# Performance work log

Hardware: AMD Instinct MI355X
Metric: run time of the kernel (lower is better)

## Reference

```python
import jax, jax.numpy as jnp
import numpy as np

NU, NI, E, DIN, D, NB, NC = 100000, 50000, 2000000, 64, 64, 2, 5


def setup_inputs() -> dict:
    key = jax.random.key(0)
    ks = jax.random.split(key, 10)
    return {
        "ufeat": jax.random.normal(ks[0], (NU, DIN), dtype=jnp.float32),
        "ifeat": jax.random.normal(ks[1], (NI, DIN), dtype=jnp.float32),
        "c_u": jax.random.uniform(ks[2], (NU, 1), dtype=jnp.float32),
        "c_i": jax.random.uniform(ks[3], (NI, 1), dtype=jnp.float32),
        "W_user": jax.random.normal(ks[4], (DIN, D), dtype=jnp.float32) * (1.0 / np.sqrt(DIN)),
        "W_item": jax.random.normal(ks[5], (DIN, D), dtype=jnp.float32) * (1.0 / np.sqrt(DIN)),
        "P": jax.random.normal(ks[6], (NB, D, D), dtype=jnp.float32) * (1.0 / np.sqrt(D)),
        "Wc": jax.random.normal(ks[7], (NC, NB), dtype=jnp.float32),
        "src": jax.random.randint(ks[8], (E,), 0, NU, dtype=jnp.int32),
        "dst": jax.random.randint(ks[9], (E,), 0, NI, dtype=jnp.int32),
    }


def reference(ufeat, ifeat, c_u, c_i, W_user, W_item, P, Wc, src, dst):
    # --- GCMCGraphConv user->item: feat @ W, scale by c_j, copy_u + sum scatter, scale by c_i ---
    msg_u = (ufeat @ W_user) * c_u                                   # [NU, D]
    h_item = jax.ops.segment_sum(msg_u[src], dst, num_segments=ifeat.shape[0]) * c_i  # [NI, D]
    # --- GCMCGraphConv item->user (reverse edges) ---
    msg_i = (ifeat @ W_item) * c_i                                   # [NI, D]
    h_user = jax.ops.segment_sum(msg_i[dst], src, num_segments=ufeat.shape[0]) * c_u  # [NU, D]
    # --- BiDecoder: per-edge bilinear dot for each basis, then basis combine ---
    hu_b = jnp.einsum('nd,sde->nse', h_user, P)                      # [NU, NB, D]
    sr = jnp.einsum('esd,ed->es', hu_b[src], h_item[dst])            # [E, NB]
    out = sr @ Wc.T                                                  # [E, NC]
    return out
```

## Files before the change

kernel.cpp:

```cpp
#include <hip/hip_runtime.h>
#include <hip/hip_fp16.h>

#define NUu 100000
#define NIi 50000
#define NEe 2000000

#define NCBI   25
#define NCBU   49
#define NCB    74
#define NBLK1  500
#define CHUNK1 4000

#define BR    16
#define NBKI  3125
#define NBKU  6250
#define CAPI  896
#define CAPU  512
#define FSUB2 8
#define FOWN2 16
#define FPC   128

__global__ __launch_bounds__(256) void gemm64_both(
    const float* __restrict__ ufeat, const float* __restrict__ ifeat,
    const float* __restrict__ W_user, const float* __restrict__ W_item,
    const float* __restrict__ c_u, const float* __restrict__ c_i,
    __half* __restrict__ msg_u, __half* __restrict__ msg_i)
{
    __shared__ float Wl[64 * 64];
    __shared__ float rows[16][64];
    const int tid  = threadIdx.x;
    const int user = (blockIdx.x < (NUu + 15) / 16) ? 1 : 0;
    const int bid  = user ? blockIdx.x : blockIdx.x - (NUu + 15) / 16;
    const float* feat = user ? ufeat : ifeat;
    const float* W    = user ? W_user : W_item;
    const float* cvec = user ? c_u : c_i;
    __half* out       = user ? msg_u : msg_i;
    const int N       = user ? NUu : NIi;

    for (int i = tid; i < 4096; i += 256) Wl[i] = W[i];
    const int r0 = bid * 16;
    for (int i = tid; i < 16 * 64; i += 256) {
        int r = r0 + (i >> 6);
        rows[i >> 6][i & 63] = (r < N) ? feat[(size_t)r * 64 + (i & 63)] : 0.f;
    }
    __syncthreads();
    const int col = tid & 63;
    const int rq  = tid >> 6;
    for (int rr = rq; rr < 16; rr += 4) {
        int r = r0 + rr;
        if (r >= N) continue;
        float s = 0.f;
        #pragma unroll
        for (int k = 0; k < 64; ++k)
            s = fmaf(rows[rr][k], Wl[k * 64 + col], s);
        out[(size_t)r * 64 + col] = __float2half(s * cvec[r]);
    }
}

__global__ __launch_bounds__(256) void hist1(
    const int* __restrict__ src, const int* __restrict__ dst, int* __restrict__ counts)
{
    __shared__ int cnt[NCB];
    const int tid = threadIdx.x;
    if (tid < NCB) cnt[tid] = 0;
    __syncthreads();
    const int beg = blockIdx.x * CHUNK1;
    for (int i = beg + tid * 4; i < beg + CHUNK1; i += 1024) {
        uint4 s4 = *(const uint4*)(src + i);
        uint4 d4 = *(const uint4*)(dst + i);
        atomicAdd(&cnt[d4.x >> 11], 1);
        atomicAdd(&cnt[d4.y >> 11], 1);
        atomicAdd(&cnt[d4.z >> 11], 1);
        atomicAdd(&cnt[d4.w >> 11], 1);
        atomicAdd(&cnt[NCBI + (s4.x >> 11)], 1);
        atomicAdd(&cnt[NCBI + (s4.y >> 11)], 1);
        atomicAdd(&cnt[NCBI + (s4.z >> 11)], 1);
        atomicAdd(&cnt[NCBI + (s4.w >> 11)], 1);
    }
    __syncthreads();
    if (tid < NCB) counts[tid * NBLK1 + blockIdx.x] = cnt[tid];
}

__global__ __launch_bounds__(256) void scan1(
    const int* __restrict__ counts, int* __restrict__ slotbase, int* __restrict__ rowptrC)
{
    __shared__ int tot[NCB], base[NCB];
    const int tid = threadIdx.x;
    if (tid < NCB) {
        int s = 0;
        for (int b = 0; b < NBLK1; ++b) s += counts[tid * NBLK1 + b];
        tot[tid] = s;
    }
    __syncthreads();
    if (tid == 0) {
        int run = 0;
        for (int c = 0; c < NCB; ++c) { base[c] = run; rowptrC[c] = run; run += tot[c]; }
        rowptrC[NCB] = run;
    }
    __syncthreads();
    if (tid < NCB) {
        int run = base[tid];
        for (int b = 0; b < NBLK1; ++b) {
            slotbase[tid * NBLK1 + b] = run;
            run += counts[tid * NBLK1 + b];
        }
    }
}

__global__ __launch_bounds__(256) void fill1(
    const int* __restrict__ src, const int* __restrict__ dst,
    const int* __restrict__ slotbase, unsigned int* __restrict__ payC)
{
    __shared__ int cur[NCB];
    const int tid = threadIdx.x;
    if (tid < NCB) cur[tid] = slotbase[tid * NBLK1 + blockIdx.x];
    __syncthreads();
    const int beg = blockIdx.x * CHUNK1;
#define F1_PROC(ss, dd)                                                     \
    {                                                                       \
        int _s = (int)(ss), _d = (int)(dd);                                 \
        int p1 = atomicAdd(&cur[_d >> 11], 1);                              \
        payC[p1] = ((unsigned)(_d & 2047) << 17) | (unsigned)_s;            \
        int p2 = atomicAdd(&cur[NCBI + (_s >> 11)], 1);                     \
        payC[p2] = ((unsigned)(_s & 2047) << 16) | (unsigned)_d;            \
    }
    for (int i = beg + tid * 4; i < beg + CHUNK1; i += 1024) {
        uint4 s4 = *(const uint4*)(src + i);
        uint4 d4 = *(const uint4*)(dst + i);
        F1_PROC(s4.x, d4.x);
        F1_PROC(s4.y, d4.y);
        F1_PROC(s4.z, d4.z);
        F1_PROC(s4.w, d4.w);
    }
#undef F1_PROC
}

__global__ __launch_bounds__(256) void fine_split2(
    const unsigned int* __restrict__ payC, const int* __restrict__ rowptrC,
    unsigned int* __restrict__ payI, int* __restrict__ cntFI,
    unsigned int* __restrict__ payU, int* __restrict__ cntFU)
{
    __shared__ int cur[FOWN2];
    const int tid = threadIdx.x;
    int bid = blockIdx.x;
    const int user = (bid >= NCBI * FSUB2) ? 1 : 0;
    if (user) bid -= NCBI * FSUB2;
    const int cbl = bid / FSUB2;
    const int sub = bid % FSUB2;
    const int c   = user ? (NCBI + cbl) : cbl;
    const int CAP = user ? CAPU : CAPI;
    unsigned int* __restrict__ payF = user ? payU : payI;
    int*          __restrict__ cntF = user ? cntFU : cntFI;

    if (tid < FOWN2) cur[tid] = 0;
    __syncthreads();

    const int beg = rowptrC[c], end = rowptrC[c + 1];
    const int a    = min(end, beg + ((4 - (beg & 3)) & 3));
    const int vend = a + ((end - a) & ~3);

#define FS_PROC(u)                                                          \
    {                                                                       \
        unsigned int _u = (u);                                              \
        int lr  = user ? (int)(_u >> 16) : (int)(_u >> 17);                 \
        int fbl = lr >> 4;                                                  \
        if ((fbl >> 4) == sub) {                                            \
            int pos = atomicAdd(&cur[fbl & 15], 1);                         \
            if (pos < CAP) {                                                \
                unsigned int g = user ? (_u & 0xffffu) : (_u & 0x1ffffu);   \
                payF[(size_t)(cbl * FPC + fbl) * CAP + pos] =               \
                    ((unsigned)(lr & 15) << 17) | g;                        \
            }                                                               \
        }                                                                   \
    }

    if (tid < a - beg) FS_PROC(payC[beg + tid]);
    for (int i = a + tid * 4; i < vend; i += 1024) {
        uint4 v = *(const uint4*)(payC + i);
        FS_PROC(v.x); FS_PROC(v.y); FS_PROC(v.z); FS_PROC(v.w);
    }
    {
        int i = vend + tid;
        if (i < end) FS_PROC(payC[i]);
    }
#undef FS_PROC

    __syncthreads();
    if (tid < FOWN2)
        cntF[cbl * FPC + sub * FOWN2 + tid] = min(cur[tid], CAP);
}

__global__ __launch_bounds__(256) void seg_both(
    const unsigned int* __restrict__ payI, const int* __restrict__ cntFI,
    const __half* __restrict__ msg_u, const float* __restrict__ c_i,
    __half2* __restrict__ h_item,
    const unsigned int* __restrict__ payU, const int* __restrict__ cntFU,
    const __half* __restrict__ msg_i, const float* __restrict__ c_u,
    __half2* __restrict__ h_user)
{
    __shared__ unsigned int sorted[CAPI];
    __shared__ float acc[BR * 64];
    __shared__ int cnt16w[4][BR];
    const int tid  = threadIdx.x;
    const int wv   = tid >> 6;
    const int user = (blockIdx.x >= NBKI) ? 1 : 0;
    const int buk  = user ? (blockIdx.x - NBKI) : blockIdx.x;
    const int CAP  = user ? CAPU : CAPI;
    const int len  = min((user ? cntFU : cntFI)[buk], CAP);
    const unsigned int* bp = (user ? payU : payI) + (size_t)buk * CAP;
    const __half2* msg2    = (const __half2*)(user ? msg_i : msg_u);
    const float* cvec      = user ? c_u : c_i;
    __half2* hout          = user ? h_user : h_item;
    const int N            = user ? NUu : NIi;

    for (int i = tid; i < BR * 64; i += 256) acc[i] = 0.f;
    if (tid < 64) ((int*)cnt16w)[tid] = 0;
    __syncthreads();
    for (int i = tid; i < len; i += 256)
        atomicAdd(&cnt16w[wv][bp[i] >> 17], 1);
    __syncthreads();
    if (tid == 0) {
        int run = 0;
        #pragma unroll
        for (int r = 0; r < BR; ++r)
            for (int w = 0; w < 4; ++w) {
                int cw = cnt16w[w][r];
                cnt16w[w][r] = run;
                run += cw;
            }
    }
    __syncthreads();
    for (int i = tid; i < len; i += 256) {
        unsigned int p = bp[i];
        int pos = atomicAdd(&cnt16w[wv][p >> 17], 1);
        sorted[pos] = p;
    }
    __syncthreads();

    const int col2  = tid & 31;
    const int half  = (tid >> 5) & 1;
    const int sid   = wv * 2 + half;
    const int chunk = (len + 7) >> 3;
    const int lo = sid * chunk;
    const int hi = min(lo + chunk, len);
    float2 facc = make_float2(0.f, 0.f);
    int crow = -1;
    for (int i = lo; i < hi; i += 8) {
        unsigned int pk[8];
        float2 vk[8];
        #pragma unroll
        for (int k = 0; k < 8; ++k)
            pk[k] = sorted[min(i + k, hi - 1)];
        #pragma unroll
        for (int k = 0; k < 8; ++k)
            vk[k] = __half22float2(msg2[(size_t)(pk[k] & 0x1ffffu) * 32 + col2]);
        #pragma unroll
        for (int k = 0; k < 8; ++k) {
            if (i + k < hi) {
                int r = (int)(pk[k] >> 17);
                if (r != crow) {
                    if (crow >= 0) {
                        atomicAdd(&acc[crow * 64 + 2 * col2],     facc.x);
                        atomicAdd(&acc[crow * 64 + 2 * col2 + 1], facc.y);
                    }
                    crow = r;
                    facc = make_float2(0.f, 0.f);
                }
                facc.x += vk[k].x;
                facc.y += vk[k].y;
            }
        }
    }
    if (crow >= 0) {
        atomicAdd(&acc[crow * 64 + 2 * col2],     facc.x);
        atomicAdd(&acc[crow * 64 + 2 * col2 + 1], facc.y);
    }
    __syncthreads();

    const int r0 = buk * BR;
    for (int idx = tid; idx < BR * 32; idx += 256) {
        int r = idx >> 5, j2 = idx & 31;
        int R = r0 + r;
        if (R < N) {
            float c = cvec[R];
            hout[(size_t)R * 32 + j2] =
                __floats2half2_rn(acc[r * 64 + 2 * j2] * c, acc[r * 64 + 2 * j2 + 1] * c);
        }
    }
}

__global__ __launch_bounds__(256) void basis_projT_h(
    const __half* __restrict__ h, const float* __restrict__ P,
    __half* __restrict__ hb, int N)
{
    __shared__ float Pl[2 * 64 * 65];
    __shared__ float rows[8][64];
    const int tid = threadIdx.x;
    for (int i = tid; i < 8192; i += 256) {
        int b = i >> 12, rem = i & 4095, dg = rem >> 6, kg = rem & 63;
        Pl[b * 4160 + kg * 65 + dg] = P[i];
    }
    const int r0 = blockIdx.x * 8;
    for (int i = tid; i < 512; i += 256) {
        int r = r0 + (i >> 6);
        rows[i >> 6][i & 63] = (r < N) ? __half2float(h[(size_t)r * 64 + (i & 63)]) : 0.f;
    }
    __syncthreads();
    const int col = tid & 63;
    const int b   = (tid >> 6) & 1;
    const int rh  = tid >> 7;
    for (int rr = rh; rr < 8; rr += 2) {
        int r = r0 + rr;
        if (r >= N) continue;
        float s = 0.f;
        #pragma unroll
        for (int k = 0; k < 64; ++k)
            s = fmaf(rows[rr][k], Pl[b * 4160 + k * 65 + col], s);
        hb[((size_t)r * 2 + b) * 64 + col] = __float2half(s);
    }
}

__global__ __launch_bounds__(256) void edge_out_h(
    const uint4* __restrict__ hu,
    const uint4* __restrict__ hib,
    const int* __restrict__ src, const int* __restrict__ dst,
    const float* __restrict__ Wc, float* __restrict__ out, int nocts)
{
    const int l   = threadIdx.x & 63;
    const int q   = l >> 3;
    const int j   = l & 7;
    const int wid = blockIdx.x * 4 + (threadIdx.x >> 6);
    const int nw  = gridDim.x * 4;
    const float wcA = (j < 5) ? Wc[2 * j]     : 0.f;
    const float wcB = (j < 5) ? Wc[2 * j + 1] : 0.f;
    for (int t = wid; t < nocts; t += nw) {
        int e = t * 8 + q;
        int s = src[e], d = dst[e];
        uint4 ua = hu[(size_t)s * 8 + j];
        uint4 b0 = hib[(size_t)d * 16 + j];
        uint4 b1 = hib[(size_t)d * 16 + 8 + j];
        float2 u0 = __half22float2(*(const __half2*)&ua.x);
        float2 u1 = __half22float2(*(const __half2*)&ua.y);
        float2 u2 = __half22float2(*(const __half2*)&ua.z);
        float2 u3 = __half22float2(*(const __half2*)&ua.w);
        float2 v0 = __half22float2(*(const __half2*)&b0.x);
        float2 v1 = __half22float2(*(const __half2*)&b0.y);
        float2 v2 = __half22float2(*(const __half2*)&b0.z);
        float2 v3 = __half22float2(*(const __half2*)&b0.w);
        float2 w0 = __half22float2(*(const __half2*)&b1.x);
        float2 w1 = __half22float2(*(const __half2*)&b1.y);
        float2 w2 = __half22float2(*(const __half2*)&b1.z);
        float2 w3 = __half22float2(*(const __half2*)&b1.w);
        float p0 = u0.x * v0.x + u0.y * v0.y + u1.x * v1.x + u1.y * v1.y
                 + u2.x * v2.x + u2.y * v2.y + u3.x * v3.x + u3.y * v3.y;
        float p1 = u0.x * w0.x + u0.y * w0.y + u1.x * w1.x + u1.y * w1.y
                 + u2.x * w2.x + u2.y * w2.y + u3.x * w3.x + u3.y * w3.y;
        #pragma unroll
        for (int m = 1; m < 8; m <<= 1) {
            p0 += __shfl_xor(p0, m, 64);
            p1 += __shfl_xor(p1, m, 64);
        }
        if (j < 5) out[(size_t)e * 5 + j] = p0 * wcA + p1 * wcB;
    }
}

extern "C" void kernel_launch(void* const* d_in, const int* in_sizes, int n_in,
                              void* d_out, int out_size, void* d_ws, size_t ws_size,
                              hipStream_t stream) {
    const float* ufeat  = (const float*)d_in[0];
    const float* ifeat  = (const float*)d_in[1];
    const float* c_u    = (const float*)d_in[2];
    const float* c_i    = (const float*)d_in[3];
    const float* W_user = (const float*)d_in[4];
    const float* W_item = (const float*)d_in[5];
    const float* P      = (const float*)d_in[6];
    const float* Wc     = (const float*)d_in[7];
    const int*   src    = (const int*)d_in[8];
    const int*   dst    = (const int*)d_in[9];
    float* out = (float*)d_out;
    char*  ws  = (char*)d_ws;

    __half*       msg_u    = (__half*)(ws);
    __half*       msg_i    = (__half*)(ws + 12800000);
    __half*       h_item   = (__half*)(ws + 19200000);
    __half*       h_user   = (__half*)(ws + 25600000);
    unsigned int* payC     = (unsigned int*)(ws + 38400000);
    __half*       hi_b     = (__half*)(ws + 38400000);
    unsigned int* payI     = (unsigned int*)(ws + 54400000);
    unsigned int* payU     = (unsigned int*)(ws + 65600000);
    int*          counts   = (int*)(ws + 78400000);
    int*          slotbase = (int*)(ws + 78551552);
    int*          rowptrC  = (int*)(ws + 78703104);
    int*          cntFI    = (int*)(ws + 78703404);
    int*          cntFU    = (int*)(ws + 78716204);

    gemm64_both<<<(NUu + 15) / 16 + (NIi + 15) / 16, 256, 0, stream>>>(
        ufeat, ifeat, W_user, W_item, c_u, c_i, msg_u, msg_i);

    hist1<<<NBLK1, 256, 0, stream>>>(src, dst, counts);
    scan1<<<1, 256, 0, stream>>>(counts, slotbase, rowptrC);
    fill1<<<NBLK1, 256, 0, stream>>>(src, dst, slotbase, payC);
    fine_split2<<<(NCBI + NCBU) * FSUB2, 256, 0, stream>>>(
        payC, rowptrC, payI, cntFI, payU, cntFU);

    seg_both<<<NBKI + NBKU, 256, 0, stream>>>(
        payI, cntFI, msg_u, c_i, (__half2*)h_item,
        payU, cntFU, msg_i, c_u, (__half2*)h_user);

    basis_projT_h<<<(NIi + 7) / 8, 256, 0, stream>>>(h_item, P, hi_b, NIi);
    edge_out_h<<<2048, 256, 0, stream>>>(
        (const uint4*)h_user, (const uint4*)hi_b, src, dst, Wc, out, NEe / 8);
}
```

Baseline: 404.6 us.

## Fuse histogram into GEMM launch, use finer coarse buckets, widen seg gathers

The edge histogram now runs in extra blocks appended to the feature GEMM launch, which removes one kernel launch and lets the two run side by side. The coarse bucket width drops from 2048 to 512 rows, so the fine split needs no sub-block filtering and each block handles a whole coarse bucket in a single pass with 32 counters. The segment-sum gather loads 4 halves (uint2) per thread across 16 streams instead of 2 halves across 8, making each load wider. The trade-offs are a larger scan (294 buckets, run serially by one block), more shared-memory atomics per row flush, and fine-split blocks that each process more edges.

Result: slower. 424.7 us (+5.0%).

```diff
diff --git a/kernel.cpp b/kernel.cpp
--- a/kernel.cpp
+++ b/kernel.cpp
@@ -5,30 +5,55 @@
 #define NIi 50000
 #define NEe 2000000
 
-#define NCBI   25
-#define NCBU   49
-#define NCB    74
+#define NCBI3  98
+#define NCBU3  196
+#define NCB3   294
 #define NBLK1  500
 #define CHUNK1 4000
+#define NGB    9375
 
 #define BR    16
 #define NBKI  3125
 #define NBKU  6250
 #define CAPI  896
 #define CAPU  512
-#define FSUB2 8
-#define FOWN2 16
-#define FPC   128
-
-__global__ __launch_bounds__(256) void gemm64_both(
+#define FPC3  32
+
+__global__ __launch_bounds__(256) void gemm_hist(
     const float* __restrict__ ufeat, const float* __restrict__ ifeat,
     const float* __restrict__ W_user, const float* __restrict__ W_item,
     const float* __restrict__ c_u, const float* __restrict__ c_i,
-    __half* __restrict__ msg_u, __half* __restrict__ msg_i)
+    __half* __restrict__ msg_u, __half* __restrict__ msg_i,
+    const int* __restrict__ src, const int* __restrict__ dst,
+    int* __restrict__ counts)
 {
     __shared__ float Wl[64 * 64];
     __shared__ float rows[16][64];
-    const int tid  = threadIdx.x;
+    __shared__ int cnt[NCB3];
+    const int tid = threadIdx.x;
+
+    if (blockIdx.x >= NGB) {
+        const int hb = blockIdx.x - NGB;
+        for (int i = tid; i < NCB3; i += 256) cnt[i] = 0;
+        __syncthreads();
+        const int beg = hb * CHUNK1;
+        for (int i = beg + tid * 4; i < beg + CHUNK1; i += 1024) {
+            uint4 s4 = *(const uint4*)(src + i);
+            uint4 d4 = *(const uint4*)(dst + i);
+            atomicAdd(&cnt[d4.x >> 9], 1);
+            atomicAdd(&cnt[d4.y >> 9], 1);
+            atomicAdd(&cnt[d4.z >> 9], 1);
+            atomicAdd(&cnt[d4.w >> 9], 1);
+            atomicAdd(&cnt[NCBI3 + (s4.x >> 9)], 1);
+            atomicAdd(&cnt[NCBI3 + (s4.y >> 9)], 1);
+            atomicAdd(&cnt[NCBI3 + (s4.z >> 9)], 1);
+            atomicAdd(&cnt[NCBI3 + (s4.w >> 9)], 1);
+        }
+        __syncthreads();
+        for (int i = tid; i < NCB3; i += 256) counts[i * NBLK1 + hb] = cnt[i];
+        return;
+    }
+
     const int user = (blockIdx.x < (NUu + 15) / 16) ? 1 : 0;
     const int bid  = user ? blockIdx.x : blockIdx.x - (NUu + 15) / 16;
     const float* feat = user ? ufeat : ifeat;
@@ -57,36 +82,12 @@
     }
 }
 
-__global__ __launch_bounds__(256) void hist1(
-    const int* __restrict__ src, const int* __restrict__ dst, int* __restrict__ counts)
-{
-    __shared__ int cnt[NCB];
+__global__ __launch_bounds__(512) void scan1(
+    const int* __restrict__ counts, int* __restrict__ slotbase, int* __restrict__ rowptrC)
+{
+    __shared__ int tot[NCB3], base[NCB3];
     const int tid = threadIdx.x;
-    if (tid < NCB) cnt[tid] = 0;
-    __syncthreads();
-    const int beg = blockIdx.x * CHUNK1;
-    for (int i = beg + tid * 4; i < beg + CHUNK1; i += 1024) {
-        uint4 s4 = *(const uint4*)(src + i);
-        uint4 d4 = *(const uint4*)(dst + i);
-        atomicAdd(&cnt[d4.x >> 11], 1);
-        atomicAdd(&cnt[d4.y >> 11], 1);
-        atomicAdd(&cnt[d4.z >> 11], 1);
-        atomicAdd(&cnt[d4.w >> 11], 1);
-        atomicAdd(&cnt[NCBI + (s4.x >> 11)], 1);
-        atomicAdd(&cnt[NCBI + (s4.y >> 11)], 1);
-        atomicAdd(&cnt[NCBI + (s4.z >> 11)], 1);
-        atomicAdd(&cnt[NCBI + (s4.w >> 11)], 1);
-    }
-    __syncthreads();
-    if (tid < NCB) counts[tid * NBLK1 + blockIdx.x] = cnt[tid];
-}
-
-__global__ __launch_bounds__(256) void scan1(
-    const int* __restrict__ counts, int* __restrict__ slotbase, int* __restrict__ rowptrC)
-{
-    __shared__ int tot[NCB], base[NCB];
-    const int tid = threadIdx.x;
-    if (tid < NCB) {
+    if (tid < NCB3) {
         int s = 0;
         for (int b = 0; b < NBLK1; ++b) s += counts[tid * NBLK1 + b];
         tot[tid] = s;
@@ -94,11 +95,11 @@
     __syncthreads();
     if (tid == 0) {
         int run = 0;
-        for (int c = 0; c < NCB; ++c) { base[c] = run; rowptrC[c] = run; run += tot[c]; }
-        rowptrC[NCB] = run;
-    }
-    __syncthreads();
-    if (tid < NCB) {
+        for (int c = 0; c < NCB3; ++c) { base[c] = run; rowptrC[c] = run; run += tot[c]; }
+        rowptrC[NCB3] = run;
+    }
+    __syncthreads();
+    if (tid < NCB3) {
         int run = base[tid];
         for (int b = 0; b < NBLK1; ++b) {
             slotbase[tid * NBLK1 + b] = run;
@@ -111,18 +112,18 @@
     const int* __restrict__ src, const int* __restrict__ dst,
     const int* __restrict__ slotbase, unsigned int* __restrict__ payC)
 {
-    __shared__ int cur[NCB];
+    __shared__ int cur[NCB3];
     const int tid = threadIdx.x;
-    if (tid < NCB) cur[tid] = slotbase[tid * NBLK1 + blockIdx.x];
+    for (int i = tid; i < NCB3; i += 256) cur[i] = slotbase[i * NBLK1 + blockIdx.x];
     __syncthreads();
     const int beg = blockIdx.x * CHUNK1;
 #define F1_PROC(ss, dd)                                                     \
     {                                                                       \
         int _s = (int)(ss), _d = (int)(dd);                                 \
-        int p1 = atomicAdd(&cur[_d >> 11], 1);                              \
-        payC[p1] = ((unsigned)(_d & 2047) << 17) | (unsigned)_s;            \
-        int p2 = atomicAdd(&cur[NCBI + (_s >> 11)], 1);                     \
-        payC[p2] = ((unsigned)(_s & 2047) << 16) | (unsigned)_d;            \
+        int p1 = atomicAdd(&cur[_d >> 9], 1);                               \
+        payC[p1] = ((unsigned)(_d & 511) << 17) | (unsigned)_s;             \
+        int p2 = atomicAdd(&cur[NCBI3 + (_s >> 9)], 1);                     \
+        payC[p2] = ((unsigned)(_s & 511) << 17) | (unsigned)_d;             \
     }
     for (int i = beg + tid * 4; i < beg + CHUNK1; i += 1024) {
         uint4 s4 = *(const uint4*)(src + i);
@@ -135,43 +136,35 @@
 #undef F1_PROC
 }
 
-__global__ __launch_bounds__(256) void fine_split2(
+__global__ __launch_bounds__(256) void fine_split3(
     const unsigned int* __restrict__ payC, const int* __restrict__ rowptrC,
     unsigned int* __restrict__ payI, int* __restrict__ cntFI,
     unsigned int* __restrict__ payU, int* __restrict__ cntFU)
 {
-    __shared__ int cur[FOWN2];
+    __shared__ int cur[FPC3];
     const int tid = threadIdx.x;
-    int bid = blockIdx.x;
-    const int user = (bid >= NCBI * FSUB2) ? 1 : 0;
-    if (user) bid -= NCBI * FSUB2;
-    const int cbl = bid / FSUB2;
-    const int sub = bid % FSUB2;
-    const int c   = user ? (NCBI + cbl) : cbl;
-    const int CAP = user ? CAPU : CAPI;
+    const int user = (blockIdx.x >= NCBI3) ? 1 : 0;
+    const int cbl  = user ? blockIdx.x - NCBI3 : blockIdx.x;
+    const int CAP  = user ? CAPU : CAPI;
     unsigned int* __restrict__ payF = user ? payU : payI;
     int*          __restrict__ cntF = user ? cntFU : cntFI;
 
-    if (tid < FOWN2) cur[tid] = 0;
-    __syncthreads();
-
-    const int beg = rowptrC[c], end = rowptrC[c + 1];
+    if (tid < FPC3) cur[tid] = 0;
+    __syncthreads();
+
+    const int beg = rowptrC[blockIdx.x], end = rowptrC[blockIdx.x + 1];
     const int a    = min(end, beg + ((4 - (beg & 3)) & 3));
     const int vend = a + ((end - a) & ~3);
 
 #define FS_PROC(u)                                                          \
     {                                                                       \
         unsigned int _u = (u);                                              \
-        int lr  = user ? (int)(_u >> 16) : (int)(_u >> 17);                 \
+        int lr  = (int)(_u >> 17);                                          \
         int fbl = lr >> 4;                                                  \
-        if ((fbl >> 4) == sub) {                                            \
-            int pos = atomicAdd(&cur[fbl & 15], 1);                         \
-            if (pos < CAP) {                                                \
-                unsigned int g = user ? (_u & 0xffffu) : (_u & 0x1ffffu);   \
-                payF[(size_t)(cbl * FPC + fbl) * CAP + pos] =               \
-                    ((unsigned)(lr & 15) << 17) | g;                        \
-            }                                                               \
-        }                                                                   \
+        int pos = atomicAdd(&cur[fbl], 1);                                  \
+        if (pos < CAP)                                                      \
+            payF[(size_t)(cbl * FPC3 + fbl) * CAP + pos] =                  \
+                ((unsigned)(lr & 15) << 17) | (_u & 0x1ffffu);              \
     }
 
     if (tid < a - beg) FS_PROC(payC[beg + tid]);
@@ -186,8 +179,8 @@
 #undef FS_PROC
 
     __syncthreads();
-    if (tid < FOWN2)
-        cntF[cbl * FPC + sub * FOWN2 + tid] = min(cur[tid], CAP);
+    if (tid < FPC3)
+        cntF[cbl * FPC3 + tid] = min(cur[tid], CAP);
 }
 
 __global__ __launch_bounds__(256) void seg_both(
@@ -208,7 +201,7 @@
     const int CAP  = user ? CAPU : CAPI;
     const int len  = min((user ? cntFU : cntFI)[buk], CAP);
     const unsigned int* bp = (user ? payU : payI) + (size_t)buk * CAP;
-    const __half2* msg2    = (const __half2*)(user ? msg_i : msg_u);
+    const uint2* msg4      = (const uint2*)(user ? msg_i : msg_u);
     const float* cvec      = user ? c_u : c_i;
     __half2* hout          = user ? h_user : h_item;
     const int N            = user ? NUu : NIi;
@@ -237,43 +230,47 @@
     }
     __syncthreads();
 
-    const int col2  = tid & 31;
-    const int half  = (tid >> 5) & 1;
-    const int sid   = wv * 2 + half;
-    const int chunk = (len + 7) >> 3;
+    const int colq  = tid & 15;
+    const int sid   = tid >> 4;
+    const int chunk = (len + 15) >> 4;
     const int lo = sid * chunk;
     const int hi = min(lo + chunk, len);
-    float2 facc = make_float2(0.f, 0.f);
+    float4 facc = make_float4(0.f, 0.f, 0.f, 0.f);
     int crow = -1;
     for (int i = lo; i < hi; i += 8) {
         unsigned int pk[8];
-        float2 vk[8];
+        uint2 mk[8];
         #pragma unroll
         for (int k = 0; k < 8; ++k)
             pk[k] = sorted[min(i + k, hi - 1)];
         #pragma unroll
         for (int k = 0; k < 8; ++k)
-            vk[k] = __half22float2(msg2[(size_t)(pk[k] & 0x1ffffu) * 32 + col2]);
+            mk[k] = msg4[(size_t)(pk[k] & 0x1ffffu) * 16 + colq];
         #pragma unroll
         for (int k = 0; k < 8; ++k) {
             if (i + k < hi) {
                 int r = (int)(pk[k] >> 17);
                 if (r != crow) {
                     if (crow >= 0) {
-                        atomicAdd(&acc[crow * 64 + 2 * col2],     facc.x);
-                        atomicAdd(&acc[crow * 64 + 2 * col2 + 1], facc.y);
+                        atomicAdd(&acc[crow * 64 + 4 * colq + 0], facc.x);
+                        atomicAdd(&acc[crow * 64 + 4 * colq + 1], facc.y);
+                        atomicAdd(&acc[crow * 64 + 4 * colq + 2], facc.z);
+                        atomicAdd(&acc[crow * 64 + 4 * colq + 3], facc.w);
                     }
                     crow = r;
-                    facc = make_float2(0.f, 0.f);
+                    facc = make_float4(0.f, 0.f, 0.f, 0.f);
                 }
-                facc.x += vk[k].x;
-                facc.y += vk[k].y;
+                float2 a = __half22float2(*(const __half2*)&mk[k].x);
+                float2 b = __half22float2(*(const __half2*)&mk[k].y);
+                facc.x += a.x; facc.y += a.y; facc.z += b.x; facc.w += b.y;
             }
         }
     }
     if (crow >= 0) {
-        atomicAdd(&acc[crow * 64 + 2 * col2],     facc.x);
-        atomicAdd(&acc[crow * 64 + 2 * col2 + 1], facc.y);
+        atomicAdd(&acc[crow * 64 + 4 * colq + 0], facc.x);
+        atomicAdd(&acc[crow * 64 + 4 * colq + 1], facc.y);
+        atomicAdd(&acc[crow * 64 + 4 * colq + 2], facc.z);
+        atomicAdd(&acc[crow * 64 + 4 * colq + 3], facc.w);
     }
     __syncthreads();
 
@@ -387,21 +384,19 @@
     unsigned int* payC     = (unsigned int*)(ws + 38400000);
     __half*       hi_b     = (__half*)(ws + 38400000);
     unsigned int* payI     = (unsigned int*)(ws + 54400000);
-    unsigned int* payU     = (unsigned int*)(ws + 65600000);
-    int*          counts   = (int*)(ws + 78400000);
-    int*          slotbase = (int*)(ws + 78551552);
-    int*          rowptrC  = (int*)(ws + 78703104);
-    int*          cntFI    = (int*)(ws + 78703404);
-    int*          cntFU    = (int*)(ws + 78716204);
-
-    gemm64_both<<<(NUu + 15) / 16 + (NIi + 15) / 16, 256, 0, stream>>>(
-        ufeat, ifeat, W_user, W_item, c_u, c_i, msg_u, msg_i);
-
-    hist1<<<NBLK1, 256, 0, stream>>>(src, dst, counts);
-    scan1<<<1, 256, 0, stream>>>(counts, slotbase, rowptrC);
+    unsigned int* payU     = (unsigned int*)(ws + 65639424);
+    int*          counts   = (int*)(ws + 78484480);
+    int*          slotbase = (int*)(ws + 79072480);
+    int*          rowptrC  = (int*)(ws + 79660480);
+    int*          cntFI    = (int*)(ws + 79661660);
+    int*          cntFU    = (int*)(ws + 79674204);
+
+    gemm_hist<<<NGB + NBLK1, 256, 0, stream>>>(
+        ufeat, ifeat, W_user, W_item, c_u, c_i, msg_u, msg_i, src, dst, counts);
+
+    scan1<<<1, 512, 0, stream>>>(counts, slotbase, rowptrC);
     fill1<<<NBLK1, 256, 0, stream>>>(src, dst, slotbase, payC);
-    fine_split2<<<(NCBI + NCBU) * FSUB2, 256, 0, stream>>>(
-        payC, rowptrC, payI, cntFI, payU, cntFU);
+    fine_split3<<<NCB3, 256, 0, stream>>>(payC, rowptrC, payI, cntFI, payU, cntFU);
 
     seg_both<<<NBKI + NBKU, 256, 0, stream>>>(
         payI, cntFI, msg_u, c_i, (__half2*)h_item,
```
